# Kernel tuning notes

Hardware: AMD Instinct MI355X
Metric: run time of the kernel (lower is better)

The kernel has to match this reference:

```python
import jax, jax.numpy as jnp
import numpy as np

D_MODEL = 1024
D_HEAD = 64


def setup_inputs() -> dict:
    key = jax.random.key(0)
    k_x, k_q, k_k, k_v, k_o = jax.random.split(key, 5)
    scale = 1.0 / np.sqrt(D_MODEL)
    residual_stream = jax.random.normal(k_x, (4, 2048, D_MODEL), dtype=jnp.float32)
    Q = scale * jax.random.normal(k_q, (D_MODEL, D_HEAD), dtype=jnp.float32)
    K = scale * jax.random.normal(k_k, (D_MODEL, D_HEAD), dtype=jnp.float32)
    V = scale * jax.random.normal(k_v, (D_MODEL, D_HEAD), dtype=jnp.float32)
    O = scale * jax.random.normal(k_o, (D_MODEL, D_HEAD), dtype=jnp.float32)
    return {"residual_stream": residual_stream, "Q": Q, "K": K, "V": V, "O": O}


def reference(residual_stream, Q, K, V, O) -> jnp.ndarray:
    # queries/keys: [B, S, d_head]
    queries = jnp.einsum('bsd,dh->bsh', residual_stream, Q)
    keys = jnp.einsum('bsd,dh->bsh', residual_stream, K)
    # NOTE: original module applies NO 1/sqrt(d_head) scaling.
    pre_attention = jnp.einsum('bqh,bkh->bqk', queries, keys)  # [B, S, S]
    S = pre_attention.shape[-1]
    causal = jnp.tril(jnp.ones((S, S), dtype=bool))
    pre_attention = jnp.where(causal[None], pre_attention, -jnp.inf)
    attention = jax.nn.softmax(pre_attention, axis=-1)
    # x = residual @ V @ O^T : [B, S, d_model]
    x = jnp.einsum('bsd,dh,eh->bse', residual_stream, V, O)
    return jnp.einsum('bqk,bke->bqe', attention, x)
```

## Files before the change

kernel.cpp:

```cpp
#include <hip/hip_runtime.h>
#include <hip/hip_bf16.h>
#include <math.h>

#define BATCH 4
#define SEQ   2048
#define DM    1024
#define DH    64
#define NROWS (BATCH*SEQ)

typedef __hip_bfloat16 bf16;
typedef __attribute__((ext_vector_type(8))) short short8;
typedef __attribute__((ext_vector_type(8))) unsigned short ushortx8;
typedef __attribute__((ext_vector_type(4))) float floatx4;

__device__ __forceinline__ ushort f2bf(float f) {
    union { bf16 h; ushort u; } cv;
    cv.h = __float2bfloat16(f);
    return cv.u;
}
__device__ __forceinline__ float bf2f(ushort u) {
    union { unsigned int i; float f; } v; v.i = ((unsigned int)u) << 16; return v.f;
}

__device__ __forceinline__ void load_lds16(const ushort* g, ushort* l) {
    __builtin_amdgcn_global_load_lds(
        (const __attribute__((address_space(1))) unsigned int*)g,
        (__attribute__((address_space(3))) unsigned int*)l, 16, 0, 0);
}

__global__ __launch_bounds__(256) void wprep_kernel(
    const float* __restrict__ Q, const float* __restrict__ K,
    const float* __restrict__ V, const float* __restrict__ O,
    ushort* __restrict__ WhT, ushort* __restrict__ WlT,
    ushort* __restrict__ Oh, ushort* __restrict__ Ol)
{
    int n = blockIdx.x;
    if (n < 192) {
        const float* W = (n < 64) ? Q : (n < 128) ? K : V;
        int c = n & 63;
        for (int k = threadIdx.x; k < DM; k += 256) {
            float w = W[k * DH + c];
            ushort hi = f2bf(w);
            WhT[n * DM + k] = hi;
            WlT[n * DM + k] = f2bf(w - bf2f(hi));
        }
    } else {
        int e0 = (n - 192) << 4;
        for (int idx = threadIdx.x; idx < 16 * DH; idx += 256) {
            int off = (e0 << 6) + idx;
            float w = O[off];
            ushort hi = f2bf(w);
            Oh[off] = hi;
            Ol[off] = f2bf(w - bf2f(hi));
        }
    }
}

__global__ __launch_bounds__(512) void qkv_fused_kernel(
    const float* __restrict__ x, const ushort* __restrict__ WhT,
    const ushort* __restrict__ WlT,
    ushort* __restrict__ qh, ushort* __restrict__ ql,
    ushort* __restrict__ kh, ushort* __restrict__ kl, ushort* __restrict__ xvP)
{
    __shared__ __align__(16) ushort Xs[2][32][34];
    __shared__ __align__(16) ushort Ws[2][192][34];
    int s0 = blockIdx.x * 32;
    int t = threadIdx.x;
    int wave = t >> 6, lane = t & 63, m_ = lane & 15, qd = lane >> 4;
    int mh = wave >> 2, cg = wave & 3;
    const floatx4 z4 = {0.f, 0.f, 0.f, 0.f};
    floatx4 accq = z4, acck = z4, accv = z4;
    int xr = t >> 4, xc = (t & 15) * 2;
    for (int k0 = 0; k0 < 1024; k0 += 32) {
        float2 v = *(const float2*)&x[(size_t)(s0 + xr) * DM + k0 + xc];
        ushort h0 = f2bf(v.x), h1 = f2bf(v.y);
        *(ushort2*)&Xs[0][xr][xc] = make_ushort2(h0, h1);
        *(ushort2*)&Xs[1][xr][xc] = make_ushort2(
            f2bf(v.x - bf2f(h0)), f2bf(v.y - bf2f(h1)));
        #pragma unroll
        for (int j = 0; j < 3; ++j) {
            int idx = t + j * 512;
            int hl = (idx >= 768);
            int r2 = idx - hl * 768;
            int n = r2 >> 2, kc = (r2 & 3) * 8;
            const ushort* src = hl ? WlT : WhT;
            *(uint4*)&Ws[hl][n][kc] = *(const uint4*)&src[n * DM + k0 + kc];
        }
        __syncthreads();
        short8 ah = *(const short8*)&Xs[0][mh * 16 + m_][qd * 8];
        short8 al = *(const short8*)&Xs[1][mh * 16 + m_][qd * 8];
        int nq = cg * 16 + m_, nk = 64 + cg * 16 + m_, nv = 128 + cg * 16 + m_;
        short8 bqh = *(const short8*)&Ws[0][nq][qd * 8];
        short8 bql = *(const short8*)&Ws[1][nq][qd * 8];
        short8 bkh = *(const short8*)&Ws[0][nk][qd * 8];
        short8 bkl = *(const short8*)&Ws[1][nk][qd * 8];
        short8 bvh = *(const short8*)&Ws[0][nv][qd * 8];
        accq = __builtin_amdgcn_mfma_f32_16x16x32_bf16(ah, bqh, accq, 0, 0, 0);
        accq = __builtin_amdgcn_mfma_f32_16x16x32_bf16(al, bqh, accq, 0, 0, 0);
        accq = __builtin_amdgcn_mfma_f32_16x16x32_bf16(ah, bql, accq, 0, 0, 0);
        acck = __builtin_amdgcn_mfma_f32_16x16x32_bf16(ah, bkh, acck, 0, 0, 0);
        acck = __builtin_amdgcn_mfma_f32_16x16x32_bf16(al, bkh, acck, 0, 0, 0);
        acck = __builtin_amdgcn_mfma_f32_16x16x32_bf16(ah, bkl, acck, 0, 0, 0);
        accv = __builtin_amdgcn_mfma_f32_16x16x32_bf16(ah, bvh, accv, 0, 0, 0);
        __syncthreads();
    }
    int col = cg * 16 + m_;
    #pragma unroll
    for (int r = 0; r < 4; ++r) {
        int row = s0 + mh * 16 + qd * 4 + r;
        ushort hq = f2bf(accq[r]);
        qh[row * 64 + col] = hq;
        ql[row * 64 + col] = f2bf(accq[r] - bf2f(hq));
        ushort hk = f2bf(acck[r]);
        kh[row * 64 + col] = hk;
        kl[row * 64 + col] = f2bf(acck[r] - bf2f(hk));
    }
    int b = s0 >> 11, c32 = (s0 & 2047) >> 5;
    ushort4 v4;
    v4.x = f2bf(accv[0]); v4.y = f2bf(accv[1]);
    v4.z = f2bf(accv[2]); v4.w = f2bf(accv[3]);
    *(ushort4*)&xvP[(size_t)(((b * 64 + c32) * 4 + qd) * 512) + col * 8 + mh * 4] = v4;
}

__global__ __launch_bounds__(512) void attn_part_kernel(
    const ushort* __restrict__ qh, const ushort* __restrict__ ql,
    const ushort* __restrict__ kh, const ushort* __restrict__ kl,
    const ushort* __restrict__ xvP,
    float* __restrict__ Opart, float* __restrict__ lpart)
{
    __shared__ __align__(16) ushort Kbuf[2][8192];
    __shared__ __align__(16) ushort xvbuf[2][4096];
    __shared__ float lred[2][2][16];
    int bid = blockIdx.x;
    int pp = bid & 63, b = (bid >> 6) & 3, s = bid >> 8;
    int srowA = pp << 4, srowB = (127 - pp) << 4;
    int t = threadIdx.x, wave = t >> 6, lane = t & 63, m_ = lane & 15, qd = lane >> 4;
    int nA = (pp >> 2) + 1, nB = ((127 - pp) >> 2) + 1;
    int tile = wave >> 2, h2 = (wave >> 1) & 1, nh = wave & 1;
    int srow = tile ? srowB : srowA;
    int nT = tile ? nB : nA;
    int jB = (nB - s + 3) >> 2;
    const ushort* khb = kh + (((size_t)b << 11)) * 64;
    const ushort* klb = kl + (((size_t)b << 11)) * 64;
    const ushort* xvPb = xvP + ((size_t)b << 17);
    short8 bq[2][2];
    {
        size_t qr = (size_t)((b << 11) + srow + m_) * 64 + qd * 8;
        bq[0][0] = *(const short8*)&qh[qr];
        bq[0][1] = *(const short8*)&qh[qr + 32];
        bq[1][0] = *(const short8*)&ql[qr];
        bq[1][1] = *(const short8*)&ql[qr + 32];
    }
    int drow = lane >> 3;
    int dlc = ((lane & 7) ^ drow) * 8;
    #define AT_STAGE(cc, buf)                                                   \
        { int k0r_ = (cc) << 6;                                                 \
          _Pragma("unroll")                                                     \
          for (int i_ = 0; i_ < 3; ++i_) {                                      \
              int c_ = wave * 3 + i_;                                           \
              if (c_ < 8)                                                       \
                  load_lds16(khb + (size_t)(k0r_ + c_ * 8 + drow) * 64 + dlc,   \
                             &Kbuf[buf][c_ * 512]);                             \
              else if (c_ < 16)                                                 \
                  load_lds16(klb + (size_t)(k0r_ + (c_ - 8) * 8 + drow) * 64 + dlc, \
                             &Kbuf[buf][4096 + (c_ - 8) * 512]);                \
              else                                                              \
                  load_lds16(xvPb + (size_t)(cc) * 4096 + (c_ - 16) * 512 + lane * 8, \
                             &xvbuf[buf][(c_ - 16) * 512]);                     \
          } }
    const floatx4 z4 = {0.f, 0.f, 0.f, 0.f};
    floatx4 accO[2] = {z4, z4};
    float ll = 0.f;
    int qrow = srow + m_;
    AT_STAGE(s, 0)
    for (int j = 0; j < jB; ++j) {
        int c = s + 4 * j;
        __syncthreads();
        if (j + 1 < jB) AT_STAGE(s + 4 * (j + 1), (j + 1) & 1)
        if (c < nT) {
            int bufi = j & 1;
            floatx4 accS[2] = {z4, z4};
            #pragma unroll
            for (int kk = 0; kk < 2; ++kk) {
                #pragma unroll
                for (int tt = 0; tt < 2; ++tt) {
                    int row = (2 * h2 + tt) * 16 + m_;
                    int chunk = ((kk << 2) + qd) ^ (m_ & 7);
                    const ushort* ph = &Kbuf[bufi][row * 64 + chunk * 8];
                    short8 akh = *(const short8*)ph;
                    short8 akl = *(const short8*)(ph + 4096);
                    accS[tt] = __builtin_amdgcn_mfma_f32_16x16x32_bf16(akh, bq[0][kk], accS[tt], 0, 0, 0);
                    accS[tt] = __builtin_amdgcn_mfma_f32_16x16x32_bf16(akl, bq[0][kk], accS[tt], 0, 0, 0);
                    accS[tt] = __builtin_amdgcn_mfma_f32_16x16x32_bf16(akh, bq[1][kk], accS[tt], 0, 0, 0);
                }
            }
            float lsum = 0.f;
            short8 pa;
            #pragma unroll
            for (int tt = 0; tt < 2; ++tt) {
                #pragma unroll
                for (int r = 0; r < 4; ++r) {
                    int kc = c * 64 + (2 * h2 + tt) * 16 + qd * 4 + r;
                    float p = (kc <= qrow) ? __expf(accS[tt][r]) : 0.f;
                    lsum += p;
                    pa[tt * 4 + r] = (short)f2bf(p);
                }
            }
            if (nh == 0) ll += lsum;
            const ushort* Xb = &xvbuf[bufi][(h2 * 4 + qd) * 512];
            #pragma unroll
            for (int i = 0; i < 2; ++i) {
                int h = (nh * 2 + i) * 16 + m_;
                short8 xv = *(const short8*)&Xb[h * 8];
                accO[i] = __builtin_amdgcn_mfma_f32_16x16x32_bf16(pa, xv, accO[i], 0, 0, 0);
            }
        }
    }
    ll += __shfl_xor(ll, 16); ll += __shfl_xor(ll, 32);
    if (qd == 0 && nh == 0) lred[tile][h2][m_] = ll;
    __syncthreads();
    if (t < 32) {
        int tl = t >> 4, q = t & 15;
        int row = (b << 11) + (tl ? srowB : srowA) + q;
        lpart[(size_t)s * NROWS + row] = lred[tl][0][q] + lred[tl][1][q];
    }
    float* OP = Opart + ((size_t)(s * 2 + h2) * NROWS + (b << 11) + srow) * 64;
    #pragma unroll
    for (int i = 0; i < 2; ++i)
        #pragma unroll
        for (int r = 0; r < 4; ++r)
            OP[(qd * 4 + r) * 64 + (nh * 2 + i) * 16 + m_] = accO[i][r];
    #undef AT_STAGE
}

__global__ __launch_bounds__(512) void out_fused_kernel(
    const float* __restrict__ Opart, const float* __restrict__ lpart,
    const ushort* __restrict__ Oh, const ushort* __restrict__ Ol,
    float* __restrict__ out)
{
    __shared__ float Axv[16][68];
    __shared__ float lsc[16];
    int r0 = blockIdx.x * 16;
    int t = threadIdx.x;
    if (t < 16) {
        int rg = r0 + t;
        lsc[t] = 1.f / (lpart[rg] + lpart[NROWS + rg]
                      + lpart[2 * NROWS + rg] + lpart[3 * NROWS + rg]);
    }
    __syncthreads();
    {
        const size_t PSL = (size_t)NROWS * DH;
        size_t e = (size_t)r0 * 64 + t * 2;
        float2 a = *(const float2*)&Opart[e];
        #pragma unroll
        for (int sp = 1; sp < 8; ++sp) {
            float2 w = *(const float2*)&Opart[sp * PSL + e];
            a.x += w.x; a.y += w.y;
        }
        int rr = t >> 5;
        float sc = lsc[rr];
        Axv[rr][(t & 31) * 2]     = a.x * sc;
        Axv[rr][(t & 31) * 2 + 1] = a.y * sc;
    }
    __syncthreads();
    int wave = t >> 6, lane = t & 63, m_ = lane & 15, qd = lane >> 4;
    int e0w = wave << 7;
    short8 Ah[2], Al[2];
    #pragma unroll
    for (int kk = 0; kk < 2; ++kk)
        #pragma unroll
        for (int j = 0; j < 8; ++j) {
            float vv = Axv[m_][kk * 32 + qd * 8 + j];
            ushort hv = f2bf(vv);
            Ah[kk][j] = (short)hv;
            Al[kk][j] = (short)f2bf(vv - bf2f(hv));
        }
    const floatx4 z4 = {0.f, 0.f, 0.f, 0.f};
    floatx4 acc[8] = {z4, z4, z4, z4, z4, z4, z4, z4};
    #pragma unroll
    for (int ni = 0; ni < 8; ++ni) {
        #pragma unroll
        for (int kk = 0; kk < 2; ++kk) {
            size_t boff = (size_t)(e0w + ni * 16 + m_) * 64 + kk * 32 + qd * 8;
            short8 bh = *(const short8*)&Oh[boff];
            short8 bl = *(const short8*)&Ol[boff];
            acc[ni] = __builtin_amdgcn_mfma_f32_16x16x32_bf16(Ah[kk], bh, acc[ni], 0, 0, 0);
            acc[ni] = __builtin_amdgcn_mfma_f32_16x16x32_bf16(Al[kk], bh, acc[ni], 0, 0, 0);
            acc[ni] = __builtin_amdgcn_mfma_f32_16x16x32_bf16(Ah[kk], bl, acc[ni], 0, 0, 0);
        }
    }
    #pragma unroll
    for (int r = 0; r < 4; ++r) {
        float* orow = out + (size_t)(r0 + qd * 4 + r) * DM + e0w;
        #pragma unroll
        for (int ni = 0; ni < 8; ++ni)
            orow[ni * 16 + m_] = acc[ni][r];
    }
}

extern "C" void kernel_launch(void* const* d_in, const int* in_sizes, int n_in,
                              void* d_out, int out_size, void* d_ws, size_t ws_size,
                              hipStream_t stream) {
    const float* x = (const float*)d_in[0];
    const float* Q = (const float*)d_in[1];
    const float* K = (const float*)d_in[2];
    const float* V = (const float*)d_in[3];
    const float* O = (const float*)d_in[4];
    float* out = (float*)d_out;

    char* ws = (char*)d_ws;
    ushort* qh   = (ushort*)(ws);
    ushort* ql   = (ushort*)(ws + (1ull  << 20));
    ushort* kh   = (ushort*)(ws + (2ull  << 20));
    ushort* kl   = (ushort*)(ws + (3ull  << 20));
    ushort* xvP  = (ushort*)(ws + (4ull  << 20));
    ushort* WhT  = (ushort*)(ws + (5ull  << 20));
    ushort* WlT  = (ushort*)(ws + (5ull  << 20) + (512ull << 10));
    float*  lpart = (float*)(ws + (6ull  << 20));
    ushort* Oh   = (ushort*)(ws + (6ull  << 20) + (256ull << 10));
    ushort* Ol   = (ushort*)(ws + (6ull  << 20) + (384ull << 10));
    float*  Opart = (float*)(ws + (7ull << 20));

    wprep_kernel<<<256, 256, 0, stream>>>(Q, K, V, O, WhT, WlT, Oh, Ol);
    qkv_fused_kernel<<<NROWS / 32, 512, 0, stream>>>(x, WhT, WlT, qh, ql, kh, kl, xvP);
    attn_part_kernel<<<64 * BATCH * 4, 512, 0, stream>>>(qh, ql, kh, kl, xvP, Opart, lpart);
    out_fused_kernel<<<NROWS / 16, 512, 0, stream>>>(Opart, lpart, Oh, Ol, out);
}
```

Before: 171.8 us.

## Double-buffer QKV projection tiles with register prefetch of next K-slice

Restructures the QKV projection main loop into a software pipeline. The next K-slice of x and the weights is loaded into registers while MFMAs run on the current LDS buffer, then written into a second LDS buffer. The LDS row padding also changes from 34 to 40. The aim is to hide global-load latency behind compute, at the cost of doubled LDS and extra registers, which may reduce occupancy. The two barriers per iteration are kept.

```diff
diff --git a/kernel.cpp b/kernel.cpp
--- a/kernel.cpp
+++ b/kernel.cpp
@@ -56,14 +56,15 @@
     }
 }
 
+#define QPAD 40
 __global__ __launch_bounds__(512) void qkv_fused_kernel(
     const float* __restrict__ x, const ushort* __restrict__ WhT,
     const ushort* __restrict__ WlT,
     ushort* __restrict__ qh, ushort* __restrict__ ql,
     ushort* __restrict__ kh, ushort* __restrict__ kl, ushort* __restrict__ xvP)
 {
-    __shared__ __align__(16) ushort Xs[2][32][34];
-    __shared__ __align__(16) ushort Ws[2][192][34];
+    __shared__ __align__(16) ushort Xs[2][2][32][QPAD];
+    __shared__ __align__(16) ushort Ws[2][2][192][QPAD];
     int s0 = blockIdx.x * 32;
     int t = threadIdx.x;
     int wave = t >> 6, lane = t & 63, m_ = lane & 15, qd = lane >> 4;
@@ -71,30 +72,48 @@
     const floatx4 z4 = {0.f, 0.f, 0.f, 0.f};
     floatx4 accq = z4, acck = z4, accv = z4;
     int xr = t >> 4, xc = (t & 15) * 2;
-    for (int k0 = 0; k0 < 1024; k0 += 32) {
-        float2 v = *(const float2*)&x[(size_t)(s0 + xr) * DM + k0 + xc];
-        ushort h0 = f2bf(v.x), h1 = f2bf(v.y);
-        *(ushort2*)&Xs[0][xr][xc] = make_ushort2(h0, h1);
-        *(ushort2*)&Xs[1][xr][xc] = make_ushort2(
-            f2bf(v.x - bf2f(h0)), f2bf(v.y - bf2f(h1)));
-        #pragma unroll
-        for (int j = 0; j < 3; ++j) {
-            int idx = t + j * 512;
-            int hl = (idx >= 768);
-            int r2 = idx - hl * 768;
-            int n = r2 >> 2, kc = (r2 & 3) * 8;
-            const ushort* src = hl ? WlT : WhT;
-            *(uint4*)&Ws[hl][n][kc] = *(const uint4*)&src[n * DM + k0 + kc];
-        }
-        __syncthreads();
-        short8 ah = *(const short8*)&Xs[0][mh * 16 + m_][qd * 8];
-        short8 al = *(const short8*)&Xs[1][mh * 16 + m_][qd * 8];
+    int widx[3], whl[3], wn[3], wkc[3];
+    #pragma unroll
+    for (int j = 0; j < 3; ++j) {
+        int idx = t + j * 512;
+        whl[j] = (idx >= 768);
+        int r2 = idx - whl[j] * 768;
+        wn[j] = r2 >> 2; wkc[j] = (r2 & 3) * 8;
+        widx[j] = wn[j] * DM + wkc[j];
+    }
+    float2 xs_reg;
+    uint4 w_reg[3];
+    xs_reg = *(const float2*)&x[(size_t)(s0 + xr) * DM + xc];
+    #pragma unroll
+    for (int j = 0; j < 3; ++j)
+        w_reg[j] = *(const uint4*)&(whl[j] ? WlT : WhT)[widx[j]];
+    {
+        ushort h0 = f2bf(xs_reg.x), h1 = f2bf(xs_reg.y);
+        *(ushort2*)&Xs[0][0][xr][xc] = make_ushort2(h0, h1);
+        *(ushort2*)&Xs[0][1][xr][xc] = make_ushort2(
+            f2bf(xs_reg.x - bf2f(h0)), f2bf(xs_reg.y - bf2f(h1)));
+        #pragma unroll
+        for (int j = 0; j < 3; ++j)
+            *(uint4*)&Ws[0][whl[j]][wn[j]][wkc[j]] = w_reg[j];
+    }
+    __syncthreads();
+    for (int it = 0; it < 32; ++it) {
+        int cur = it & 1;
+        if (it < 31) {
+            int k0n = (it + 1) * 32;
+            xs_reg = *(const float2*)&x[(size_t)(s0 + xr) * DM + k0n + xc];
+            #pragma unroll
+            for (int j = 0; j < 3; ++j)
+                w_reg[j] = *(const uint4*)&(whl[j] ? WlT : WhT)[widx[j] + k0n];
+        }
+        short8 ah = *(const short8*)&Xs[cur][0][mh * 16 + m_][qd * 8];
+        short8 al = *(const short8*)&Xs[cur][1][mh * 16 + m_][qd * 8];
         int nq = cg * 16 + m_, nk = 64 + cg * 16 + m_, nv = 128 + cg * 16 + m_;
-        short8 bqh = *(const short8*)&Ws[0][nq][qd * 8];
-        short8 bql = *(const short8*)&Ws[1][nq][qd * 8];
-        short8 bkh = *(const short8*)&Ws[0][nk][qd * 8];
-        short8 bkl = *(const short8*)&Ws[1][nk][qd * 8];
-        short8 bvh = *(const short8*)&Ws[0][nv][qd * 8];
+        short8 bqh = *(const short8*)&Ws[cur][0][nq][qd * 8];
+        short8 bql = *(const short8*)&Ws[cur][1][nq][qd * 8];
+        short8 bkh = *(const short8*)&Ws[cur][0][nk][qd * 8];
+        short8 bkl = *(const short8*)&Ws[cur][1][nk][qd * 8];
+        short8 bvh = *(const short8*)&Ws[cur][0][nv][qd * 8];
         accq = __builtin_amdgcn_mfma_f32_16x16x32_bf16(ah, bqh, accq, 0, 0, 0);
         accq = __builtin_amdgcn_mfma_f32_16x16x32_bf16(al, bqh, accq, 0, 0, 0);
         accq = __builtin_amdgcn_mfma_f32_16x16x32_bf16(ah, bql, accq, 0, 0, 0);
@@ -102,6 +121,17 @@
         acck = __builtin_amdgcn_mfma_f32_16x16x32_bf16(al, bkh, acck, 0, 0, 0);
         acck = __builtin_amdgcn_mfma_f32_16x16x32_bf16(ah, bkl, acck, 0, 0, 0);
         accv = __builtin_amdgcn_mfma_f32_16x16x32_bf16(ah, bvh, accv, 0, 0, 0);
+        __syncthreads();
+        if (it < 31) {
+            int nxt = cur ^ 1;
+            ushort h0 = f2bf(xs_reg.x), h1 = f2bf(xs_reg.y);
+            *(ushort2*)&Xs[nxt][0][xr][xc] = make_ushort2(h0, h1);
+            *(ushort2*)&Xs[nxt][1][xr][xc] = make_ushort2(
+                f2bf(xs_reg.x - bf2f(h0)), f2bf(xs_reg.y - bf2f(h1)));
+            #pragma unroll
+            for (int j = 0; j < 3; ++j)
+                *(uint4*)&Ws[nxt][whl[j]][wn[j]][wkc[j]] = w_reg[j];
+        }
         __syncthreads();
     }
     int col = cg * 16 + m_;
```

Result: slower. 195.1 us (+13.6%).
